# Performance work log

Measured on AMD Instinct MI355X. Metric: run time of the kernel, lower is better.

Reference implementation:

```python
import jax, jax.numpy as jnp
import numpy as np

N = 50000      # nodes
E = 160000     # edges
NFEAT = 1024
NHID = 512
NCLASS = 64


def _unif(k, shape, fan):
    s = 1.0 / np.sqrt(fan)
    return jax.random.uniform(k, shape, jnp.float32, -s, s)


def setup_inputs() -> dict:
    key = jax.random.key(0)
    ks = jax.random.split(key, 16)
    x = jax.random.normal(ks[0], (N, NFEAT), jnp.float32)
    adj_row = jax.random.randint(ks[1], (E,), 0, N, jnp.int32)
    adj_col = jax.random.randint(ks[2], (E,), 0, N, jnp.int32)
    adj_val = jax.random.uniform(ks[3], (E,), jnp.float32)
    # gc1: nfeat -> nhid (stdv = 1/sqrt(out_features))
    W1 = _unif(ks[4], (NFEAT, NHID), NHID)
    b1 = _unif(ks[5], (NHID,), NHID)
    # residual projection for gc1 (nn.Linear nfeat->nhid)
    p1W = _unif(ks[6], (NFEAT, NHID), NFEAT)
    p1b = _unif(ks[7], (NHID,), NFEAT)
    # gc3: nhid -> nhid (shared across 4 applications)
    W3 = _unif(ks[8], (NHID, NHID), NHID)
    b3 = _unif(ks[9], (NHID,), NHID)
    # gc2: nhid -> nclass
    W2 = _unif(ks[10], (NHID, NCLASS), NCLASS)
    b2 = _unif(ks[11], (NCLASS,), NCLASS)
    # residual projection for gc2 (nn.Linear nhid->nclass)
    p2W = _unif(ks[12], (NHID, NCLASS), NHID)
    p2b = _unif(ks[13], (NCLASS,), NHID)
    return {"x": x, "adj_row": adj_row, "adj_col": adj_col, "adj_val": adj_val,
            "W1": W1, "b1": b1, "p1W": p1W, "p1b": p1b,
            "W3": W3, "b3": b3, "W2": W2, "b2": b2, "p2W": p2W, "p2b": p2b}


def _spmm(row, col, val, support):
    # out[i] = sum_e val[e] * support[col[e]] for row[e] == i   (adj @ support)
    return jax.ops.segment_sum(val[:, None] * support[col], row, num_segments=N)


def reference(x, adj_row, adj_col, adj_val, W1, b1, p1W, p1b, W3, b3, W2, b2, p2W, p2b):
    def gc_proj(inp, W, b, pW, pb):
        # shapes differ -> projected residual
        out = _spmm(adj_row, adj_col, adj_val, inp @ W) + b
        return jax.nn.relu(out + inp @ pW + pb)

    def gc_res(inp, W, b):
        # same shape -> identity residual
        out = _spmm(adj_row, adj_col, adj_val, inp @ W) + b
        return jax.nn.relu(out + inp)

    h = jax.nn.relu(gc_proj(x, W1, b1, p1W, p1b))       # [N, NHID]
    for _ in range(4):                                   # gc3 shared weights x4
        h = jax.nn.relu(gc_res(h, W3, b3))
    h = gc_proj(h, W2, b2, p2W, p2b)                     # [N, NCLASS]
    return jax.nn.log_softmax(h, axis=1)
```

## Files before the change

### kernel.cpp

```cpp
#include <hip/hip_runtime.h>

typedef __attribute__((ext_vector_type(8))) short bf16x8;
typedef __attribute__((ext_vector_type(8))) unsigned short ushort8;
typedef __attribute__((ext_vector_type(4))) float f32x4;

#define NNODES 50000
#define NEDGES 160000
#define MP     50048
#define NB_SCAN 196

__device__ __forceinline__ float bf2f(unsigned short u) {
  return __uint_as_float(((unsigned int)u) << 16);
}
__device__ __forceinline__ unsigned short f2bf(float f) {
  unsigned int u = __float_as_uint(f);
  u += 0x7fffu + ((u >> 16) & 1u);
  return (unsigned short)(u >> 16);
}
__device__ __forceinline__ void gld16(const void* g, void* l) {
  __builtin_amdgcn_global_load_lds((__attribute__((address_space(1))) void*)g,
                                   (__attribute__((address_space(3))) void*)l, 16, 0, 0);
}

__global__ void k_hist(const int* __restrict__ row, int* __restrict__ cnt, int n) {
  int i = blockIdx.x * 256 + threadIdx.x;
  if (i < n) atomicAdd(&cnt[row[i]], 1);
}

__global__ void k_block_reduce(const int* __restrict__ cnt, int* __restrict__ bsum, int n) {
  __shared__ int sd[256];
  int i = blockIdx.x * 256 + threadIdx.x;
  sd[threadIdx.x] = (i < n) ? cnt[i] : 0;
  __syncthreads();
  for (int o = 128; o > 0; o >>= 1) {
    if (threadIdx.x < o) sd[threadIdx.x] += sd[threadIdx.x + o];
    __syncthreads();
  }
  if (threadIdx.x == 0) bsum[blockIdx.x] = sd[0];
}

__global__ void k_scan_bsum(const int* __restrict__ bsum, int* __restrict__ boff, int nb,
                            int* __restrict__ rowptr, int n, int E) {
  __shared__ int sd[256];
  int v = (threadIdx.x < nb) ? bsum[threadIdx.x] : 0;
  sd[threadIdx.x] = v;
  __syncthreads();
  for (int o = 1; o < 256; o <<= 1) {
    int t = (threadIdx.x >= o) ? sd[threadIdx.x - o] : 0;
    __syncthreads();
    sd[threadIdx.x] += t;
    __syncthreads();
  }
  if (threadIdx.x < nb) boff[threadIdx.x] = sd[threadIdx.x] - v;
  if (threadIdx.x == 0) rowptr[n] = E;
}

__global__ void k_block_scan(const int* __restrict__ cnt, const int* __restrict__ boff,
                             int* __restrict__ rowptr, int* __restrict__ cursor, int n) {
  __shared__ int sd[256];
  int i = blockIdx.x * 256 + threadIdx.x;
  int v = (i < n) ? cnt[i] : 0;
  sd[threadIdx.x] = v;
  __syncthreads();
  for (int o = 1; o < 256; o <<= 1) {
    int t = (threadIdx.x >= o) ? sd[threadIdx.x - o] : 0;
    __syncthreads();
    sd[threadIdx.x] += t;
    __syncthreads();
  }
  if (i < n) {
    int r = boff[blockIdx.x] + sd[threadIdx.x] - v;
    rowptr[i] = r;
    cursor[i] = r;
  }
}

__global__ void k_scatter(const int* __restrict__ row, const int* __restrict__ col,
                          const float* __restrict__ val, int* __restrict__ cursor,
                          int* __restrict__ scol, float* __restrict__ sval, int n) {
  int e = blockIdx.x * 256 + threadIdx.x;
  if (e < n) {
    int p = atomicAdd(&cursor[row[e]], 1);
    scol[p] = col[e];
    sval[p] = val[e];
  }
}

__global__ void k_cast_x(const float* __restrict__ x, unsigned short* __restrict__ xb, int nRealRows) {
  size_t idx = ((size_t)blockIdx.x * 256 + threadIdx.x) * 8;
  if (idx >= (size_t)MP * 1024) return;
  int row = (int)(idx >> 10);
  ushort8 o;
  if (row < nRealRows) {
    float4 a = *(const float4*)(x + idx);
    float4 b = *(const float4*)(x + idx + 4);
    o[0] = f2bf(a.x); o[1] = f2bf(a.y); o[2] = f2bf(a.z); o[3] = f2bf(a.w);
    o[4] = f2bf(b.x); o[5] = f2bf(b.y); o[6] = f2bf(b.z); o[7] = f2bf(b.w);
  } else {
    o = (ushort8){0,0,0,0,0,0,0,0};
  }
  *(ushort8*)(xb + idx) = o;
}

__global__ void k_packT(const float* __restrict__ src, int K, int srcW, int nc,
                        unsigned short* __restrict__ dst, int dstOff) {
  __shared__ float tile[32][33];
  int k0 = blockIdx.x * 32, n0 = blockIdx.y * 32;
  int tx = threadIdx.x, ty = threadIdx.y;
  for (int i = ty; i < 32; i += 8)
    tile[i][tx] = src[(size_t)(k0 + i) * srcW + (n0 + tx)];
  __syncthreads();
  for (int i = ty; i < 32; i += 8)
    dst[(size_t)(dstOff + n0 + i) * K + (k0 + tx)] = f2bf(tile[tx][i]);
}

__global__ void k_pack_bias(const float* __restrict__ b1, const float* __restrict__ p1b,
                            const float* __restrict__ b2, const float* __restrict__ p2b,
                            float* __restrict__ bias1, float* __restrict__ bias2) {
  int t = threadIdx.x;
  bias1[t] = b1[t] + p1b[t];
  if (t < 64) bias2[t] = b2[t] + p2b[t];
}

__global__ __launch_bounds__(256) void k_gemm_bt(
    const unsigned short* __restrict__ A, const unsigned short* __restrict__ Bt,
    unsigned short* __restrict__ C, int M, int N, int K) {
  __shared__ __align__(16) unsigned short As[128 * 32];
  __shared__ __align__(16) unsigned short Bs[128 * 32];
  const int ntc = N >> 7;
  const int mt = blockIdx.x / ntc;
  const int nt = blockIdx.x % ntc;
  const int t = threadIdx.x;
  const int w = t >> 6, lane = t & 63;
  const int wr = w >> 1, wc = w & 1;
  f32x4 acc[4][4] = {};
  const unsigned short* ga = A + (size_t)(mt * 128 + (t >> 2)) * K + (t & 3) * 8;
  const unsigned short* gb = Bt + (size_t)(nt * 128 + (t >> 2)) * K + (t & 3) * 8;
  unsigned short* lA = &As[w * 512];
  unsigned short* lB = &Bs[w * 512];
  const size_t rowskip = (size_t)64 * K;
  for (int kt = 0; kt < K; kt += 32) {
    gld16(ga + kt, lA);
    gld16(ga + kt + rowskip, lA + 2048);
    gld16(gb + kt, lB);
    gld16(gb + kt + rowskip, lB + 2048);
    __syncthreads();
    bf16x8 af[4], bfr[4];
#pragma unroll
    for (int m = 0; m < 4; ++m)
      af[m] = *(const bf16x8*)&As[(wr * 64 + m * 16 + (lane & 15)) * 32 + (lane >> 4) * 8];
#pragma unroll
    for (int n = 0; n < 4; ++n)
      bfr[n] = *(const bf16x8*)&Bs[(wc * 64 + n * 16 + (lane & 15)) * 32 + (lane >> 4) * 8];
#pragma unroll
    for (int m = 0; m < 4; ++m)
#pragma unroll
      for (int n = 0; n < 4; ++n)
        acc[m][n] = __builtin_amdgcn_mfma_f32_16x16x32_bf16(af[m], bfr[n], acc[m][n], 0, 0, 0);
    __syncthreads();
  }
  const int r0 = mt * 128 + wr * 64 + (lane >> 4) * 4;
  const int c0 = nt * 128 + wc * 64 + (lane & 15);
#pragma unroll
  for (int m = 0; m < 4; ++m)
#pragma unroll
    for (int n = 0; n < 4; ++n)
#pragma unroll
      for (int r = 0; r < 4; ++r)
        C[(size_t)(r0 + m * 16 + r) * N + (c0 + n * 16)] = f2bf(acc[m][n][r]);
}

__global__ __launch_bounds__(256) void k_spmm_ep512(
    const int* __restrict__ rowptr, const int* __restrict__ scol, const float* __restrict__ sval,
    const unsigned short* __restrict__ s, int sStride,
    const unsigned short* __restrict__ res, int resStride,
    const float* __restrict__ bias,
    unsigned short* __restrict__ o, int oStride, int nReal, int nTot) {
  int gw = (blockIdx.x * 256 + threadIdx.x) >> 6;
  int lane = threadIdx.x & 63;
  if (gw >= nTot) return;
  unsigned short* op = o + (size_t)gw * oStride + lane * 8;
  if (gw >= nReal) {
    *(ushort8*)op = (ushort8){0,0,0,0,0,0,0,0};
    return;
  }
  float acc[8] = {0.f,0.f,0.f,0.f,0.f,0.f,0.f,0.f};
  int e0 = rowptr[gw], e1 = rowptr[gw + 1];
  for (int e = e0; e < e1; ++e) {
    int c = scol[e];
    float v = sval[e];
    ushort8 svv = *(const ushort8*)(s + (size_t)c * sStride + lane * 8);
#pragma unroll
    for (int k = 0; k < 8; ++k) acc[k] += v * bf2f(svv[k]);
  }
  ushort8 rv = *(const ushort8*)(res + (size_t)gw * resStride + lane * 8);
  ushort8 ov;
#pragma unroll
  for (int k = 0; k < 8; ++k) {
    float tt = acc[k] + bias[lane * 8 + k] + bf2f(rv[k]);
    ov[k] = f2bf(fmaxf(tt, 0.f));
  }
  *(ushort8*)op = ov;
}

__global__ __launch_bounds__(256) void k_spmm_lsm(
    const int* __restrict__ rowptr, const int* __restrict__ scol, const float* __restrict__ sval,
    const unsigned short* __restrict__ g2, const float* __restrict__ bias2,
    float* __restrict__ out, int n) {
  int gw = (blockIdx.x * 256 + threadIdx.x) >> 6;
  int lane = threadIdx.x & 63;
  if (gw >= n) return;
  int e0 = rowptr[gw], e1 = rowptr[gw + 1];
  float acc = 0.f;
  for (int e = e0; e < e1; ++e) {
    int c = scol[e];
    acc += sval[e] * bf2f(g2[(size_t)c * 128 + lane]);
  }
  float t = acc + bias2[lane] + bf2f(g2[(size_t)gw * 128 + 64 + lane]);
  float v = fmaxf(t, 0.f);
  float m = v;
#pragma unroll
  for (int o = 32; o > 0; o >>= 1) m = fmaxf(m, __shfl_xor(m, o));
  float ex = __expf(v - m);
  float ss = ex;
#pragma unroll
  for (int o = 32; o > 0; o >>= 1) ss += __shfl_xor(ss, o);
  out[(size_t)gw * 64 + lane] = v - m - __logf(ss);
}

extern "C" void kernel_launch(void* const* d_in, const int* in_sizes, int n_in,
                              void* d_out, int out_size, void* d_ws, size_t ws_size,
                              hipStream_t stream) {
  const float* x    = (const float*)d_in[0];
  const int*   arow = (const int*)d_in[1];
  const int*   acol = (const int*)d_in[2];
  const float* aval = (const float*)d_in[3];
  const float* W1   = (const float*)d_in[4];
  const float* b1   = (const float*)d_in[5];
  const float* p1W  = (const float*)d_in[6];
  const float* p1b  = (const float*)d_in[7];
  const float* W3   = (const float*)d_in[8];
  const float* b3   = (const float*)d_in[9];
  const float* W2   = (const float*)d_in[10];
  const float* b2   = (const float*)d_in[11];
  const float* p2W  = (const float*)d_in[12];
  const float* p2b  = (const float*)d_in[13];
  float* out = (float*)d_out;

  char* wsp = (char*)d_ws;
  size_t off = 0;
  auto take = [&](size_t bytes) -> char* {
    char* p = wsp + off;
    off = (off + bytes + 255) & ~(size_t)255;
    return p;
  };
  unsigned short* xb  = (unsigned short*)take((size_t)MP * 1024 * 2);
  unsigned short* g1  = (unsigned short*)take((size_t)MP * 1024 * 2);
  unsigned short* B1t = (unsigned short*)take((size_t)1024 * 1024 * 2);
  unsigned short* W3t = (unsigned short*)take((size_t)512 * 512 * 2);
  unsigned short* B2t = (unsigned short*)take((size_t)128 * 512 * 2);
  float* bias1 = (float*)take(512 * 4);
  float* bias2 = (float*)take(64 * 4);
  int*   cnt    = (int*)take((size_t)NNODES * 4);
  int*   rowptr = (int*)take((size_t)(NNODES + 1) * 4);
  int*   bsum   = (int*)take(256 * 4);
  int*   boff   = (int*)take(256 * 4);
  int*   scol   = (int*)take((size_t)NEDGES * 4);
  float* sval   = (float*)take((size_t)NEDGES * 4);
  unsigned short* h  = xb;
  unsigned short* s  = g1;
  unsigned short* g2 = g1;

  hipMemsetAsync(cnt, 0, (size_t)NNODES * 4, stream);
  k_hist<<<(NEDGES + 255) / 256, 256, 0, stream>>>(arow, cnt, NEDGES);
  k_block_reduce<<<NB_SCAN, 256, 0, stream>>>(cnt, bsum, NNODES);
  k_scan_bsum<<<1, 256, 0, stream>>>(bsum, boff, NB_SCAN, rowptr, NNODES, NEDGES);
  k_block_scan<<<NB_SCAN, 256, 0, stream>>>(cnt, boff, rowptr, cnt, NNODES);
  k_scatter<<<(NEDGES + 255) / 256, 256, 0, stream>>>(arow, acol, aval, cnt, scol, sval, NEDGES);

  k_cast_x<<<(int)(((size_t)MP * 1024 / 8 + 255) / 256), 256, 0, stream>>>(x, xb, NNODES);
  k_packT<<<dim3(1024 / 32, 512 / 32), dim3(32, 8), 0, stream>>>(W1, 1024, 512, 512, B1t, 0);
  k_packT<<<dim3(1024 / 32, 512 / 32), dim3(32, 8), 0, stream>>>(p1W, 1024, 512, 512, B1t, 512);
  k_packT<<<dim3(512 / 32, 512 / 32), dim3(32, 8), 0, stream>>>(W3, 512, 512, 512, W3t, 0);
  k_packT<<<dim3(512 / 32, 64 / 32), dim3(32, 8), 0, stream>>>(W2, 512, 64, 64, B2t, 0);
  k_packT<<<dim3(512 / 32, 64 / 32), dim3(32, 8), 0, stream>>>(p2W, 512, 64, 64, B2t, 64);
  k_pack_bias<<<1, 512, 0, stream>>>(b1, p1b, b2, p2b, bias1, bias2);

  k_gemm_bt<<<391 * 8, 256, 0, stream>>>(xb, B1t, g1, MP, 1024, 1024);
  k_spmm_ep512<<<MP / 4, 256, 0, stream>>>(rowptr, scol, sval, g1, 1024, g1 + 512, 1024,
                                           bias1, h, 512, NNODES, MP);
  for (int i = 0; i < 4; ++i) {
    k_gemm_bt<<<391 * 4, 256, 0, stream>>>(h, W3t, s, MP, 512, 512);
    k_spmm_ep512<<<MP / 4, 256, 0, stream>>>(rowptr, scol, sval, s, 512, h, 512,
                                             b3, h, 512, NNODES, MP);
  }
  k_gemm_bt<<<391, 256, 0, stream>>>(h, B2t, g2, MP, 128, 512);
  k_spmm_lsm<<<(NNODES + 3) / 4, 256, 0, stream>>>(rowptr, scol, sval, g2, bias2, out, NNODES);
}
```

Measured before the change: 699.0 us.

## Add 128x256 triple-buffered GEMM with XCD swizzle for the wide projections

Adds a new 512-thread GEMM kernel with 128x256 tiles, a three-stage global_load_lds pipeline, an XOR-swizzled LDS layout and an XCD-aware block remapping. It replaces the 128x128 GEMM for the 1024-wide and 512-wide layers. Row padding grows so M divides evenly into 128 rows for the new grid. The aim is more operand reuse per tile, better latency hiding and better L2 locality. In exchange it uses 72KB of dynamic LDS per block, which limits occupancy.

```diff
diff --git a/kernel.cpp b/kernel.cpp
--- a/kernel.cpp
+++ b/kernel.cpp
@@ -6,7 +6,7 @@
 
 #define NNODES 50000
 #define NEDGES 160000
-#define MP     50048
+#define MP     50176
 #define NB_SCAN 196
 
 __device__ __forceinline__ float bf2f(unsigned short u) {
@@ -120,6 +120,79 @@
   int t = threadIdx.x;
   bias1[t] = b1[t] + p1b[t];
   if (t < 64) bias2[t] = b2[t] + p2b[t];
+}
+
+__global__ __launch_bounds__(512, 4) void k_gemm128x256(
+    const unsigned short* __restrict__ A, const unsigned short* __restrict__ Bt,
+    unsigned short* __restrict__ C, int M, int N, int K) {
+  extern __shared__ char smem[];
+  const int NT = N >> 8;
+  const int nwg = gridDim.x;
+  const int q = nwg >> 3, r = nwg & 7;
+  const int xcd = blockIdx.x & 7, local = blockIdx.x >> 3;
+  const int swz = (xcd < r ? xcd * (q + 1) : r * (q + 1) + (xcd - r) * q) + local;
+  const int mt = swz / NT, nt = swz % NT;
+
+  const int tid = threadIdx.x;
+  const int w = tid >> 6, lane = tid & 63;
+  const int wr = w >> 2, wc = w & 3;
+
+  const int srow = tid >> 2;
+  const int schunk = (tid & 3) ^ ((tid >> 3) & 3);
+  const unsigned short* gA = A + (size_t)(mt * 128 + srow) * K + schunk * 8;
+  const unsigned short* gB = Bt + (size_t)(nt * 256 + srow) * K + schunk * 8;
+  const size_t rs128 = (size_t)128 * K;
+  const int wb = w << 10;
+
+  const int l15 = lane & 15;
+  const int cpos = ((lane >> 4) ^ ((l15 >> 1) & 3)) << 4;
+  const int aOff = (wr * 64 + l15) * 64 + cpos;
+  const int bOff = 8192 + (wc * 64 + l15) * 64 + cpos;
+
+  f32x4 acc[4][4] = {};
+  const int T = K >> 5;
+
+  auto STAGE = [&](int t) {
+    char* db = smem + (t % 3) * 24576 + wb;
+    const unsigned short* a = gA + t * 32;
+    const unsigned short* b = gB + t * 32;
+    gld16(a, db);
+    gld16(b, db + 8192);
+    gld16(b + rs128, db + 16384);
+  };
+
+  STAGE(0); STAGE(1);
+
+  for (int t = 0; t < T; ++t) {
+    if (t < T - 1) asm volatile("s_waitcnt vmcnt(3)" ::: "memory");
+    else           asm volatile("s_waitcnt vmcnt(0)" ::: "memory");
+    __builtin_amdgcn_s_barrier();
+    __builtin_amdgcn_sched_barrier(0);
+    if (t + 2 < T) STAGE(t + 2);
+    const int bb = (t % 3) * 24576;
+    bf16x8 af[4];
+#pragma unroll
+    for (int m = 0; m < 4; ++m) af[m] = *(const bf16x8*)(smem + bb + aOff + m * 1024);
+    __builtin_amdgcn_s_setprio(1);
+#pragma unroll
+    for (int n = 0; n < 4; ++n) {
+      bf16x8 bfr = *(const bf16x8*)(smem + bb + bOff + n * 1024);
+#pragma unroll
+      for (int m = 0; m < 4; ++m)
+        acc[m][n] = __builtin_amdgcn_mfma_f32_16x16x32_bf16(af[m], bfr, acc[m][n], 0, 0, 0);
+    }
+    __builtin_amdgcn_s_setprio(0);
+  }
+
+  const int r0 = mt * 128 + wr * 64 + (lane >> 4) * 4;
+  const int c0e = nt * 256 + wc * 64 + l15;
+#pragma unroll
+  for (int m = 0; m < 4; ++m)
+#pragma unroll
+    for (int n = 0; n < 4; ++n)
+#pragma unroll
+      for (int j = 0; j < 4; ++j)
+        C[(size_t)(r0 + m * 16 + j) * N + (c0e + n * 16)] = f2bf(acc[m][n][j]);
 }
 
 __global__ __launch_bounds__(256) void k_gemm_bt(
@@ -286,14 +359,14 @@
   k_packT<<<dim3(512 / 32, 64 / 32), dim3(32, 8), 0, stream>>>(p2W, 512, 64, 64, B2t, 64);
   k_pack_bias<<<1, 512, 0, stream>>>(b1, p1b, b2, p2b, bias1, bias2);
 
-  k_gemm_bt<<<391 * 8, 256, 0, stream>>>(xb, B1t, g1, MP, 1024, 1024);
+  k_gemm128x256<<<392 * 4, 512, 73728, stream>>>(xb, B1t, g1, MP, 1024, 1024);
   k_spmm_ep512<<<MP / 4, 256, 0, stream>>>(rowptr, scol, sval, g1, 1024, g1 + 512, 1024,
                                            bias1, h, 512, NNODES, MP);
   for (int i = 0; i < 4; ++i) {
-    k_gemm_bt<<<391 * 4, 256, 0, stream>>>(h, W3t, s, MP, 512, 512);
+    k_gemm128x256<<<392 * 2, 512, 73728, stream>>>(h, W3t, s, MP, 512, 512);
     k_spmm_ep512<<<MP / 4, 256, 0, stream>>>(rowptr, scol, sval, s, 512, h, 512,
                                              b3, h, 512, NNODES, MP);
   }
-  k_gemm_bt<<<391, 256, 0, stream>>>(h, B2t, g2, MP, 128, 512);
+  k_gemm_bt<<<MP / 128, 256, 0, stream>>>(h, B2t, g2, MP, 128, 512);
   k_spmm_lsm<<<(NNODES + 3) / 4, 256, 0, stream>>>(rowptr, scol, sval, g2, bias2, out, NNODES);
 }
```

Result: faster. 614.6 us (-12.1%).
